# Kernel optimization log

Hardware: AMD Instinct MI355X
Metric: run time of the kernel (lower is better)

The kernel has to match this reference:

```python
import jax, jax.numpy as jnp
import numpy as np
from jax import lax

IMG = 800.0
PRE_NMS = 2000
POST_NMS = 1000
IOU_T = 0.7
BBOX_XFORM_CLIP = float(np.log(1000.0 / 16.0))


def build_anchors():
    # torchvision FPN anchor generator: one size per level, 3 aspect ratios
    strides = [4, 8, 16, 32, 64]
    sizes = [32, 64, 128, 256, 512]
    ratios = [0.5, 1.0, 2.0]
    out = []
    for s, sz in zip(strides, sizes):
        f = int(np.ceil(800 / s))  # feature map side
        base = []
        for r in ratios:
            w = sz * np.sqrt(1.0 / r)
            h = sz * np.sqrt(r)
            base.append([-w / 2, -h / 2, w / 2, h / 2])
        base = np.asarray(base)  # [3,4]
        sx = (np.arange(f) + 0.5) * s
        sy = (np.arange(f) + 0.5) * s
        yy, xx = np.meshgrid(sy, sx, indexing='ij')
        shifts = np.stack([xx, yy, xx, yy], -1).reshape(-1, 1, 4)
        out.append((shifts + base).reshape(-1, 4))
    return np.concatenate(out, 0).astype(np.float32)  # [159882,4]


def setup_inputs() -> dict:
    key = jax.random.key(0)
    k1, k2 = jax.random.split(key)
    B = 16
    anchors = jnp.asarray(build_anchors())
    A = anchors.shape[0]
    scores = jax.random.normal(k1, (B, A), dtype=jnp.float32)
    deltas = jax.random.normal(k2, (B, A, 4), dtype=jnp.float32) * 0.1
    return {"scores": scores, "deltas": deltas, "anchors": anchors}


def decode_boxes(deltas, anchors):
    wa = anchors[:, 2] - anchors[:, 0]
    ha = anchors[:, 3] - anchors[:, 1]
    cxa = anchors[:, 0] + 0.5 * wa
    cya = anchors[:, 1] + 0.5 * ha
    dx, dy = deltas[:, 0], deltas[:, 1]
    dw = jnp.minimum(deltas[:, 2], BBOX_XFORM_CLIP)
    dh = jnp.minimum(deltas[:, 3], BBOX_XFORM_CLIP)
    cx = dx * wa + cxa
    cy = dy * ha + cya
    w = jnp.exp(dw) * wa
    h = jnp.exp(dh) * ha
    boxes = jnp.stack([cx - 0.5 * w, cy - 0.5 * h, cx + 0.5 * w, cy + 0.5 * h], -1)
    return jnp.clip(boxes, 0.0, IMG)


def box_iou(a, b):
    # a: [N,4], b: [M,4]
    area_a = (a[:, 2] - a[:, 0]) * (a[:, 3] - a[:, 1])
    area_b = (b[:, 2] - b[:, 0]) * (b[:, 3] - b[:, 1])
    lt = jnp.maximum(a[:, None, :2], b[None, :, :2])
    rb = jnp.minimum(a[:, None, 2:], b[None, :, 2:])
    wh = jnp.clip(rb - lt, 0.0)
    inter = wh[..., 0] * wh[..., 1]
    return inter / (area_a[:, None] + area_b[None, :] - inter + 1e-9)


def greedy_nms_keep(boxes, iou_t):
    # boxes are sorted by descending score
    K = boxes.shape[0]
    iou = box_iou(boxes, boxes)  # [K,K]
    idx = jnp.arange(K)

    def body(i, keep):
        sup = (iou[i] > iou_t) & keep[i] & (idx > i)
        return keep & ~sup

    return lax.fori_loop(0, K, body, jnp.ones((K,), bool))


def _process_image(scores_i, deltas_i, anchors):
    # top-k pre-NMS on objectness logits (torchvision RPN order)
    top_logits, idx = lax.top_k(scores_i, PRE_NMS)
    boxes = decode_boxes(deltas_i[idx], anchors[idx])  # [PRE,4]
    keep = greedy_nms_keep(boxes, IOU_T)
    masked = jnp.where(keep, top_logits, -jnp.inf)
    kept_logits, idx2 = lax.top_k(masked, POST_NMS)
    kept_boxes = boxes[idx2]
    valid = jnp.isfinite(kept_logits)
    probs = jax.nn.sigmoid(jnp.where(valid, kept_logits, 0.0))
    out_boxes = jnp.where(valid[:, None], kept_boxes, 0.0)
    out_scores = jnp.where(valid, probs, 0.0)
    return jnp.concatenate([out_boxes, out_scores[:, None]], -1)  # [POST,5]


def reference(scores, deltas, anchors):
    return jax.vmap(_process_image, in_axes=(0, 0, None))(scores, deltas, anchors)
```

## Files before the change

### kernel.cpp

```cpp
#include <hip/hip_runtime.h>
#include <math.h>

#define PRE_NMS 2000
#define POST_NMS 1000
#define IOU_T 0.7f
#define IMGSZ 800.0f
#define CAP 6144
#define SORTN 2048
#define NBINS 1024
#define NWORDS 32
#define NSLICE 16
#define MROWS 2048

typedef unsigned long long u64;

__device__ __forceinline__ unsigned key_of(float f) {
    unsigned u = __float_as_uint(f);
    return (u & 0x80000000u) ? ~u : (u | 0x80000000u);
}
__device__ __forceinline__ float inv_key(unsigned k) {
    unsigned u = (k & 0x80000000u) ? (k ^ 0x80000000u) : ~k;
    return __uint_as_float(u);
}

__global__ __launch_bounds__(256) void hist_kernel(
    const float* __restrict__ scores, int A, unsigned* __restrict__ ghist) {
  int b = blockIdx.x, slice = blockIdx.y;
  __shared__ unsigned h[NBINS];
  int tid = threadIdx.x;
  for (int i = tid; i < NBINS; i += 256) h[i] = 0;
  __syncthreads();
  int per = (A + NSLICE - 1) / NSLICE;
  int lo = slice * per, hi = min(lo + per, A);
  const float* sc = scores + (size_t)b * A;
  for (int i = lo + tid; i < hi; i += 256)
    atomicAdd(&h[key_of(sc[i]) >> 22], 1u);
  __syncthreads();
  for (int i = tid; i < NBINS; i += 256)
    if (h[i]) atomicAdd(&ghist[b * NBINS + i], h[i]);
}

__global__ __launch_bounds__(256) void compact_kernel(
    const float* __restrict__ scores, int A, const unsigned* __restrict__ ghist,
    u64* __restrict__ cand, int* __restrict__ cand_cnt, int* __restrict__ T1) {
  int b = blockIdx.x, slice = blockIdx.y;
  int tid = threadIdx.x;
  int lane = tid & 63, wave = tid >> 6;
  __shared__ unsigned sa[2][NBINS];
  __shared__ int sT;
  for (int i = tid; i < NBINS; i += 256) sa[0][i] = ghist[b * NBINS + i];
  __syncthreads();
  int src = 0;
  for (int d = 1; d < NBINS; d <<= 1) {
    for (int i = tid; i < NBINS; i += 256)
      sa[src ^ 1][i] = sa[src][i] + ((i + d < NBINS) ? sa[src][i + d] : 0u);
    __syncthreads();
    src ^= 1;
  }
  for (int i = tid; i < NBINS; i += 256) {
    unsigned v = sa[src][i];
    unsigned nx = (i < NBINS - 1) ? sa[src][i + 1] : 0u;
    if (v >= PRE_NMS && nx < PRE_NMS) sT = i;
  }
  __syncthreads();
  int T = sT;
  if (slice == 0 && tid == 0) T1[b] = T;
  int per = (A + NSLICE - 1) / NSLICE;
  int lo = slice * per, hi = min(lo + per, A);
  const float* sc = scores + (size_t)b * A;
  int cnt = 0;
  for (int i = lo + tid; i < hi; i += 256)
    cnt += ((int)(key_of(sc[i]) >> 22) >= T);
  int pfx = cnt;
  #pragma unroll
  for (int d = 1; d < 64; d <<= 1) {
    int t2 = __shfl_up(pfx, d, 64);
    if (lane >= d) pfx += t2;
  }
  __shared__ int s_wt[4];
  __shared__ int s_base;
  if (lane == 63) s_wt[wave] = pfx;
  __syncthreads();
  if (tid == 0) {
    int tot = s_wt[0] + s_wt[1] + s_wt[2] + s_wt[3];
    int acc = 0;
    #pragma unroll
    for (int w2 = 0; w2 < 4; ++w2) { int t3 = s_wt[w2]; s_wt[w2] = acc; acc += t3; }
    s_base = atomicAdd(&cand_cnt[b], tot);
  }
  __syncthreads();
  int my_off = s_base + s_wt[wave] + (pfx - cnt);
  u64* cb = cand + (size_t)b * CAP;
  for (int i = lo + tid; i < hi; i += 256) {
    unsigned k = key_of(sc[i]);
    if ((int)(k >> 22) >= T) {
      if (my_off < CAP) cb[my_off] = ((u64)k << 32) | (unsigned)(~i);
      my_off++;
    }
  }
}

__global__ __launch_bounds__(1024) void refine_select_kernel(
    const u64* __restrict__ cand, const int* __restrict__ cand_cnt,
    const int* __restrict__ T1,
    u64* __restrict__ gsel, int* __restrict__ sel_cnt) {
  int b = blockIdx.x, tid = threadIdx.x;
  int lane = tid & 63;
  __shared__ unsigned h2[NBINS];
  __shared__ unsigned tmp[NBINS];
  __shared__ int s_above, s_sel, s_T2;
  int n = min(cand_cnt[b], CAP);
  const u64* cb = cand + (size_t)b * CAP;
  h2[tid] = 0;
  if (tid == 0) { s_above = 0; s_sel = 0; }
  __syncthreads();
  int T1v = T1[b];
  int loc = 0;
  for (int i = tid; i < n; i += 1024) {
    unsigned k = (unsigned)(cb[i] >> 32);
    if ((int)(k >> 22) > T1v) loc++;
    else atomicAdd(&h2[(k >> 12) & 1023], 1u);
  }
  for (int d = 32; d; d >>= 1) loc += __shfl_down(loc, d, 64);
  if (lane == 0 && loc) atomicAdd(&s_above, loc);
  __syncthreads();
  unsigned v = h2[tid];
  for (int d = 1; d < NBINS; d <<= 1) {
    tmp[tid] = v;
    __syncthreads();
    if (tid + d < NBINS) v += tmp[tid + d];
    __syncthreads();
  }
  tmp[tid] = v;
  __syncthreads();
  int above = s_above;
  unsigned nextv = (tid < NBINS - 1) ? tmp[tid + 1] : 0u;
  if (above + (int)v >= PRE_NMS && above + (int)nextv < PRE_NMS) s_T2 = tid;
  __syncthreads();
  unsigned thresh20 = ((unsigned)T1v << 10) | (unsigned)s_T2;
  u64* gs = gsel + (size_t)b * SORTN;
  for (int i = tid; i < n; i += 1024) {
    u64 cv = cb[i];
    if ((unsigned)(cv >> 44) >= thresh20) {
      int pos = atomicAdd(&s_sel, 1);
      if (pos < SORTN) gs[pos] = cv;
    }
  }
  __syncthreads();
  if (tid == 0) sel_cnt[b] = min(s_sel, SORTN);
}

__global__ __launch_bounds__(256) void rank_decode_kernel(
    const u64* __restrict__ gsel, const int* __restrict__ sel_cnt,
    const float* __restrict__ deltas, const float* __restrict__ anchors, int A,
    float* __restrict__ boxes, float* __restrict__ topk_logit) {
  int b = blockIdx.x, ci = blockIdx.y;
  int tid = threadIdx.x;
  __shared__ u64 keys[SORTN];
  __shared__ int s_part[256];
  const u64* gs = gsel + (size_t)b * SORTN;
  int n = sel_cnt[b];
  for (int i = tid; i < SORTN; i += 256)
    keys[i] = (i < n) ? gs[i] : 0ULL;
  __syncthreads();
  int half = tid >> 7;
  int li = tid & 127;
  int i = ci * 128 + li;
  u64 my = keys[i];
  int rank = 0;
  const ulonglong2* k2 = (const ulonglong2*)(keys + half * (SORTN / 2));
  #pragma unroll 4
  for (int j = 0; j < SORTN / 4; ++j) {
    ulonglong2 kk = k2[j];
    rank += (kk.x > my) + (kk.y > my);
  }
  s_part[tid] = rank;
  __syncthreads();
  if (half == 0) {
    rank = s_part[tid] + s_part[tid + 128];
    if (i < n && rank < PRE_NMS) {
      int a = (int)(~(unsigned)my);
      topk_logit[b * PRE_NMS + rank] = inv_key((unsigned)(my >> 32));
      const float CLIP = 4.135166556742356f;
      float4 dl = ((const float4*)deltas)[(size_t)b * A + a];
      float4 an = ((const float4*)anchors)[a];
      float wa = __fsub_rn(an.z, an.x);
      float ha = __fsub_rn(an.w, an.y);
      float cxa = __fadd_rn(an.x, __fmul_rn(0.5f, wa));
      float cya = __fadd_rn(an.y, __fmul_rn(0.5f, ha));
      float dw = fminf(dl.z, CLIP), dh = fminf(dl.w, CLIP);
      float cx = __fadd_rn(__fmul_rn(dl.x, wa), cxa);
      float cy = __fadd_rn(__fmul_rn(dl.y, ha), cya);
      float w2 = __fmul_rn((float)exp((double)dw), wa);
      float h2f = __fmul_rn((float)exp((double)dh), ha);
      float x1 = __fsub_rn(cx, __fmul_rn(0.5f, w2));
      float y1 = __fsub_rn(cy, __fmul_rn(0.5f, h2f));
      float x2 = __fadd_rn(cx, __fmul_rn(0.5f, w2));
      float y2 = __fadd_rn(cy, __fmul_rn(0.5f, h2f));
      x1 = fminf(fmaxf(x1, 0.f), IMGSZ);
      y1 = fminf(fmaxf(y1, 0.f), IMGSZ);
      x2 = fminf(fmaxf(x2, 0.f), IMGSZ);
      y2 = fminf(fmaxf(y2, 0.f), IMGSZ);
      ((float4*)boxes)[(size_t)b * PRE_NMS + rank] = make_float4(x1, y1, x2, y2);
    }
  }
}

__global__ __launch_bounds__(64) void iou_tile(
    const float* __restrict__ boxes, u64* __restrict__ maskT) {
  int k = blockIdx.x;
  int b = blockIdx.y;
  int wj = (int)((sqrtf(8.0f * k + 1.0f) - 1.0f) * 0.5f);
  while ((wj + 1) * (wj + 2) / 2 <= k) ++wj;
  while (wj * (wj + 1) / 2 > k) --wj;
  int ti = k - wj * (wj + 1) / 2;
  int lane = threadIdx.x;
  int i = ti * 64 + lane;
  const float4* bb = (const float4*)boxes + (size_t)b * PRE_NMS;
  __shared__ float4 sbox[64];
  int jg = wj * 64 + lane;
  sbox[lane] = bb[min(jg, PRE_NMS - 1)];
  float4 A4 = bb[min(i, PRE_NMS - 1)];
  __syncthreads();
  float area_a = __fmul_rn(__fsub_rn(A4.z, A4.x), __fsub_rn(A4.w, A4.y));
  u64 m = 0;
  #pragma unroll 8
  for (int jj = 0; jj < 64; ++jj) {
    float4 Bb = sbox[jj];
    float area_b = __fmul_rn(__fsub_rn(Bb.z, Bb.x), __fsub_rn(Bb.w, Bb.y));
    float ltx = fmaxf(A4.x, Bb.x), lty = fmaxf(A4.y, Bb.y);
    float rbx = fminf(A4.z, Bb.z), rby = fminf(A4.w, Bb.w);
    float iw = fmaxf(__fsub_rn(rbx, ltx), 0.f);
    float ih = fmaxf(__fsub_rn(rby, lty), 0.f);
    float inter = __fmul_rn(iw, ih);
    float denom = __fadd_rn(__fsub_rn(__fadd_rn(area_a, area_b), inter), 1e-9f);
    float iou = inter / denom;
    int j = wj * 64 + jj;
    if (j > i && iou > IOU_T) m |= 1ULL << jj;
  }
  maskT[((size_t)b * NWORDS + wj) * MROWS + i] = m;
}

#define WSTRIDE 65
#define BAR_LDS() asm volatile("s_waitcnt lgkmcnt(0)\n\ts_barrier" ::: "memory")
__global__ __launch_bounds__(256, 1) void nms_scan(
    const u64* __restrict__ maskT, const float* __restrict__ boxes,
    const float* __restrict__ logits, float* __restrict__ out) {
  int b = blockIdx.x;
  int tid = threadIdx.x;
  int wave = tid >> 6, lane = tid & 63;
  __shared__ u64 buf[3][NWORDS * WSTRIDE];
  __shared__ u64 s_keep[NWORDS];
  __shared__ u64 s_cur[2];
  if (tid < NWORDS) s_keep[tid] = (tid == NWORDS - 1) ? 0xFFFFULL : ~0ULL;
  const u64* mb = maskT + (size_t)b * NWORDS * MROWS;
  int w = tid >> 3;
  int sub = tid & 7;
  uint4 nx0, nx1, nx2, nx3;
  {
    const uint4* src = (const uint4*)(mb + (size_t)w * MROWS + sub * 8);
    uint4 a0 = src[0], a1 = src[1], a2 = src[2], a3 = src[3];
    u64* dst = &buf[0][w * WSTRIDE + sub * 8];
    dst[0] = ((u64)a0.y << 32) | a0.x;  dst[1] = ((u64)a0.w << 32) | a0.z;
    dst[2] = ((u64)a1.y << 32) | a1.x;  dst[3] = ((u64)a1.w << 32) | a1.z;
    dst[4] = ((u64)a2.y << 32) | a2.x;  dst[5] = ((u64)a2.w << 32) | a2.z;
    dst[6] = ((u64)a3.y << 32) | a3.x;  dst[7] = ((u64)a3.w << 32) | a3.z;
  }
  if (w >= 1) {
    const uint4* src = (const uint4*)(mb + (size_t)w * MROWS + 64 + sub * 8);
    nx0 = src[0]; nx1 = src[1]; nx2 = src[2]; nx3 = src[3];
  }
  BAR_LDS();
  for (int c = 0; c < NWORDS; ++c) {
    if (c + 1 < NWORDS && w >= c + 1) {
      u64* dst = &buf[(c + 1) % 3][w * WSTRIDE + sub * 8];
      dst[0] = ((u64)nx0.y << 32) | nx0.x;  dst[1] = ((u64)nx0.w << 32) | nx0.z;
      dst[2] = ((u64)nx1.y << 32) | nx1.x;  dst[3] = ((u64)nx1.w << 32) | nx1.z;
      dst[4] = ((u64)nx2.y << 32) | nx2.x;  dst[5] = ((u64)nx2.w << 32) | nx2.z;
      dst[6] = ((u64)nx3.y << 32) | nx3.x;  dst[7] = ((u64)nx3.w << 32) | nx3.z;
    }
    if (c + 2 < NWORDS && w >= c + 2) {
      const uint4* src = (const uint4*)(mb + (size_t)w * MROWS + (c + 2) * 64 + sub * 8);
      nx0 = src[0]; nx1 = src[1]; nx2 = src[2]; nx3 = src[3];
    }
    if (wave == 0) {
      u64 diag = buf[c % 3][c * WSTRIDE + lane];
      unsigned dlo = (unsigned)diag, dhi = (unsigned)(diag >> 32);
      u64 k0 = s_keep[c];
      unsigned clo = __builtin_amdgcn_readfirstlane((unsigned)k0);
      unsigned chi = __builtin_amdgcn_readfirstlane((unsigned)(k0 >> 32));
      #pragma unroll
      for (int bb = 0; bb < 32; ++bb) {
        unsigned rlo = __builtin_amdgcn_readlane(dlo, bb);
        unsigned rhi = __builtin_amdgcn_readlane(dhi, bb);
        unsigned msk = 0u - ((clo >> bb) & 1u);
        clo &= ~(rlo & msk);
        chi &= ~(rhi & msk);
      }
      #pragma unroll
      for (int bb = 0; bb < 32; ++bb) {
        unsigned rlo = __builtin_amdgcn_readlane(dlo, bb + 32);
        unsigned rhi = __builtin_amdgcn_readlane(dhi, bb + 32);
        unsigned msk = 0u - ((chi >> bb) & 1u);
        clo &= ~(rlo & msk);
        chi &= ~(rhi & msk);
      }
      u64 cur = ((u64)chi << 32) | clo;
      if (lane == 0) { s_keep[c] = cur; s_cur[c & 1] = cur; }
      if (c + 1 < NWORDS) {
        u64 row = buf[c % 3][(c + 1) * WSTRIDE + lane];
        u64 bit = (cur >> lane) & 1ULL;
        u64 v = row & (0ULL - bit);
        v |= __shfl_xor(v, 1, 64);
        v |= __shfl_xor(v, 2, 64);
        v |= __shfl_xor(v, 4, 64);
        v |= __shfl_xor(v, 8, 64);
        v |= __shfl_xor(v, 16, 64);
        v |= __shfl_xor(v, 32, 64);
        if (lane == 0 && v) atomicAnd(&s_keep[c + 1], ~v);
      }
    } else if (c >= 1) {
      u64 kept = s_cur[(c - 1) & 1];
      int g = lane >> 3, s = lane & 7;
      const u64* bbuf = &buf[(c - 1) % 3][0];
      for (int idx = (wave - 1) + 3 * g; idx < NWORDS - 1 - c; idx += 24) {
        int w2 = c + 1 + idx;
        u64 v = 0;
        #pragma unroll
        for (int k = 0; k < 8; ++k) {
          int r = s + 8 * k;
          u64 bit = (kept >> r) & 1ULL;
          v |= bbuf[w2 * WSTRIDE + r] & (0ULL - bit);
        }
        v |= __shfl_xor(v, 1, 64);
        v |= __shfl_xor(v, 2, 64);
        v |= __shfl_xor(v, 4, 64);
        if (s == 0 && v) atomicAnd(&s_keep[w2], ~v);
      }
    }
    BAR_LDS();
  }
  __shared__ int pre[NWORDS];
  __shared__ int s_tot;
  if (tid == 0) {
    int acc = 0;
    for (int ww = 0; ww < NWORDS; ++ww) {
      pre[ww] = acc;
      acc += __popcll(s_keep[ww]);
    }
    s_tot = acc;
  }
  __syncthreads();
  const float* lg_b = logits + b * PRE_NMS;
  const float4* bx_b = (const float4*)boxes + (size_t)b * PRE_NMS;
  for (int i = tid; i < PRE_NMS; i += 256) {
    u64 wv = s_keep[i >> 6];
    if ((wv >> (i & 63)) & 1) {
      int rank = pre[i >> 6] + __popcll(wv & ((1ULL << (i & 63)) - 1ULL));
      if (rank < POST_NMS) {
        float4 bx = bx_b[i];
        float lg = lg_b[i];
        float e = (float)exp(-(double)lg);
        float pp = 1.0f / (1.0f + e);
        float* o = out + ((size_t)b * POST_NMS + rank) * 5;
        o[0] = bx.x; o[1] = bx.y; o[2] = bx.z; o[3] = bx.w; o[4] = pp;
      }
    }
  }
  int tot = s_tot;
  for (int j = tid; j < POST_NMS; j += 256) {
    if (j >= tot) {
      float* o = out + ((size_t)b * POST_NMS + j) * 5;
      o[0] = 0.f; o[1] = 0.f; o[2] = 0.f; o[3] = 0.f; o[4] = 0.f;
    }
  }
}

extern "C" void kernel_launch(void* const* d_in, const int* in_sizes, int n_in,
                              void* d_out, int out_size, void* d_ws, size_t ws_size,
                              hipStream_t stream) {
  const float* scores  = (const float*)d_in[0];
  const float* deltas  = (const float*)d_in[1];
  const float* anchors = (const float*)d_in[2];
  int A = in_sizes[2] / 4;
  int B = in_sizes[0] / A;

  char* ws = (char*)d_ws;
  size_t off = 0;
  auto alloc = [&](size_t bytes) {
    void* p = ws + off;
    off += (bytes + 255) & ~(size_t)255;
    return p;
  };
  unsigned* ghist    = (unsigned*)alloc((size_t)B * NBINS * 4);
  int*      cand_cnt = (int*)alloc((size_t)B * 4);
  size_t zero_bytes = off;
  int*      T1       = (int*)alloc((size_t)B * 4);
  u64*      cand     = (u64*)alloc((size_t)B * CAP * 8);
  u64*      gsel     = (u64*)alloc((size_t)B * SORTN * 8);
  int*      sel_cnt  = (int*)alloc((size_t)B * 4);
  float*    topk_lg  = (float*)alloc((size_t)B * PRE_NMS * 4);
  float*    boxes    = (float*)alloc((size_t)B * PRE_NMS * 16);
  u64*      maskT    = (u64*)alloc((size_t)B * NWORDS * MROWS * 8);

  hipMemsetAsync(ws, 0, zero_bytes, stream);

  hist_kernel<<<dim3(B, NSLICE), 256, 0, stream>>>(scores, A, ghist);
  compact_kernel<<<dim3(B, NSLICE), 256, 0, stream>>>(scores, A, ghist, cand, cand_cnt, T1);
  refine_select_kernel<<<B, 1024, 0, stream>>>(cand, cand_cnt, T1, gsel, sel_cnt);
  rank_decode_kernel<<<dim3(B, SORTN / 128), 256, 0, stream>>>(
      gsel, sel_cnt, deltas, anchors, A, boxes, topk_lg);
  int ntiles = NWORDS * (NWORDS + 1) / 2;
  iou_tile<<<dim3(ntiles, B), 64, 0, stream>>>(boxes, maskT);
  nms_scan<<<B, 256, 0, stream>>>(maskT, boxes, topk_lg, (float*)d_out);
}
```

Baseline: 225.1 us.

## Skip empty IoU mask tiles in NMS scan using per-tile occupancy flags

The IoU tile kernel now writes a per-tile flag saying whether any bit in the 64x64 suppression tile is set. The NMS scan loads these flags into shared memory and uses them to skip global loads of empty tiles, the serial diagonal readlane reduction, and the off-diagonal OR-reductions. This aims to cut memory traffic and serial work on the latency-bound scan, since most tiles of random boxes are empty. It adds an extra flag buffer, its writes, and flag lookups in the inner loop.

```diff
diff --git a/kernel.cpp b/kernel.cpp
--- a/kernel.cpp
+++ b/kernel.cpp
@@ -11,6 +11,7 @@
 #define NWORDS 32
 #define NSLICE 16
 #define MROWS 2048
+#define NTILES 528
 
 typedef unsigned long long u64;
 
@@ -207,7 +208,8 @@
 }
 
 __global__ __launch_bounds__(64) void iou_tile(
-    const float* __restrict__ boxes, u64* __restrict__ maskT) {
+    const float* __restrict__ boxes, u64* __restrict__ maskT,
+    unsigned* __restrict__ tflag) {
   int k = blockIdx.x;
   int b = blockIdx.y;
   int wj = (int)((sqrtf(8.0f * k + 1.0f) - 1.0f) * 0.5f);
@@ -239,12 +241,15 @@
     if (j > i && iou > IOU_T) m |= 1ULL << jj;
   }
   maskT[((size_t)b * NWORDS + wj) * MROWS + i] = m;
+  u64 anyb = __ballot(m != 0ULL);
+  if (lane == 0) tflag[(size_t)b * NTILES + k] = (anyb != 0ULL) ? 1u : 0u;
 }
 
 #define WSTRIDE 65
 #define BAR_LDS() asm volatile("s_waitcnt lgkmcnt(0)\n\ts_barrier" ::: "memory")
 __global__ __launch_bounds__(256, 1) void nms_scan(
-    const u64* __restrict__ maskT, const float* __restrict__ boxes,
+    const u64* __restrict__ maskT, const unsigned* __restrict__ tflag,
+    const float* __restrict__ boxes,
     const float* __restrict__ logits, float* __restrict__ out) {
   int b = blockIdx.x;
   int tid = threadIdx.x;
@@ -252,6 +257,10 @@
   __shared__ u64 buf[3][NWORDS * WSTRIDE];
   __shared__ u64 s_keep[NWORDS];
   __shared__ u64 s_cur[2];
+  __shared__ unsigned char sflag[NTILES];
+  const unsigned* tf = tflag + (size_t)b * NTILES;
+  for (int i2 = tid; i2 < NTILES; i2 += 256)
+    sflag[i2] = (unsigned char)(tf[i2] != 0u);
   if (tid < NWORDS) s_keep[tid] = (tid == NWORDS - 1) ? 0xFFFFULL : ~0ULL;
   const u64* mb = maskT + (size_t)b * NWORDS * MROWS;
   int w = tid >> 3;
@@ -266,48 +275,57 @@
     dst[4] = ((u64)a2.y << 32) | a2.x;  dst[5] = ((u64)a2.w << 32) | a2.z;
     dst[6] = ((u64)a3.y << 32) | a3.x;  dst[7] = ((u64)a3.w << 32) | a3.z;
   }
-  if (w >= 1) {
+  bool have = (w >= 1);
+  if (have) {
     const uint4* src = (const uint4*)(mb + (size_t)w * MROWS + 64 + sub * 8);
     nx0 = src[0]; nx1 = src[1]; nx2 = src[2]; nx3 = src[3];
   }
   BAR_LDS();
   for (int c = 0; c < NWORDS; ++c) {
-    if (c + 1 < NWORDS && w >= c + 1) {
+    if (c + 1 < NWORDS && have) {
       u64* dst = &buf[(c + 1) % 3][w * WSTRIDE + sub * 8];
       dst[0] = ((u64)nx0.y << 32) | nx0.x;  dst[1] = ((u64)nx0.w << 32) | nx0.z;
       dst[2] = ((u64)nx1.y << 32) | nx1.x;  dst[3] = ((u64)nx1.w << 32) | nx1.z;
       dst[4] = ((u64)nx2.y << 32) | nx2.x;  dst[5] = ((u64)nx2.w << 32) | nx2.z;
       dst[6] = ((u64)nx3.y << 32) | nx3.x;  dst[7] = ((u64)nx3.w << 32) | nx3.z;
     }
-    if (c + 2 < NWORDS && w >= c + 2) {
+    have = false;
+    if (c + 2 < NWORDS && w >= c + 2 &&
+        sflag[(w * (w + 1)) / 2 + (c + 2)]) {
       const uint4* src = (const uint4*)(mb + (size_t)w * MROWS + (c + 2) * 64 + sub * 8);
       nx0 = src[0]; nx1 = src[1]; nx2 = src[2]; nx3 = src[3];
+      have = true;
     }
     if (wave == 0) {
-      u64 diag = buf[c % 3][c * WSTRIDE + lane];
-      unsigned dlo = (unsigned)diag, dhi = (unsigned)(diag >> 32);
       u64 k0 = s_keep[c];
-      unsigned clo = __builtin_amdgcn_readfirstlane((unsigned)k0);
-      unsigned chi = __builtin_amdgcn_readfirstlane((unsigned)(k0 >> 32));
-      #pragma unroll
-      for (int bb = 0; bb < 32; ++bb) {
-        unsigned rlo = __builtin_amdgcn_readlane(dlo, bb);
-        unsigned rhi = __builtin_amdgcn_readlane(dhi, bb);
-        unsigned msk = 0u - ((clo >> bb) & 1u);
-        clo &= ~(rlo & msk);
-        chi &= ~(rhi & msk);
+      u64 cur;
+      if (sflag[(c * (c + 3)) >> 1]) {
+        u64 diag = buf[c % 3][c * WSTRIDE + lane];
+        unsigned dlo = (unsigned)diag, dhi = (unsigned)(diag >> 32);
+        unsigned clo = __builtin_amdgcn_readfirstlane((unsigned)k0);
+        unsigned chi = __builtin_amdgcn_readfirstlane((unsigned)(k0 >> 32));
+        #pragma unroll
+        for (int bb = 0; bb < 32; ++bb) {
+          unsigned rlo = __builtin_amdgcn_readlane(dlo, bb);
+          unsigned rhi = __builtin_amdgcn_readlane(dhi, bb);
+          unsigned msk = 0u - ((clo >> bb) & 1u);
+          clo &= ~(rlo & msk);
+          chi &= ~(rhi & msk);
+        }
+        #pragma unroll
+        for (int bb = 0; bb < 32; ++bb) {
+          unsigned rlo = __builtin_amdgcn_readlane(dlo, bb + 32);
+          unsigned rhi = __builtin_amdgcn_readlane(dhi, bb + 32);
+          unsigned msk = 0u - ((chi >> bb) & 1u);
+          clo &= ~(rlo & msk);
+          chi &= ~(rhi & msk);
+        }
+        cur = ((u64)chi << 32) | clo;
+      } else {
+        cur = k0;
       }
-      #pragma unroll
-      for (int bb = 0; bb < 32; ++bb) {
-        unsigned rlo = __builtin_amdgcn_readlane(dlo, bb + 32);
-        unsigned rhi = __builtin_amdgcn_readlane(dhi, bb + 32);
-        unsigned msk = 0u - ((chi >> bb) & 1u);
-        clo &= ~(rlo & msk);
-        chi &= ~(rhi & msk);
-      }
-      u64 cur = ((u64)chi << 32) | clo;
       if (lane == 0) { s_keep[c] = cur; s_cur[c & 1] = cur; }
-      if (c + 1 < NWORDS) {
+      if (c + 1 < NWORDS && sflag[(((c + 1) * (c + 2)) >> 1) + c]) {
         u64 row = buf[c % 3][(c + 1) * WSTRIDE + lane];
         u64 bit = (cur >> lane) & 1ULL;
         u64 v = row & (0ULL - bit);
@@ -325,6 +343,7 @@
       const u64* bbuf = &buf[(c - 1) % 3][0];
       for (int idx = (wave - 1) + 3 * g; idx < NWORDS - 1 - c; idx += 24) {
         int w2 = c + 1 + idx;
+        if (!sflag[(w2 * (w2 + 1)) / 2 + (c - 1)]) continue;
         u64 v = 0;
         #pragma unroll
         for (int k = 0; k < 8; ++k) {
@@ -402,6 +421,7 @@
   float*    topk_lg  = (float*)alloc((size_t)B * PRE_NMS * 4);
   float*    boxes    = (float*)alloc((size_t)B * PRE_NMS * 16);
   u64*      maskT    = (u64*)alloc((size_t)B * NWORDS * MROWS * 8);
+  unsigned* tflag    = (unsigned*)alloc((size_t)B * NTILES * 4);
 
   hipMemsetAsync(ws, 0, zero_bytes, stream);
 
@@ -410,7 +430,7 @@
   refine_select_kernel<<<B, 1024, 0, stream>>>(cand, cand_cnt, T1, gsel, sel_cnt);
   rank_decode_kernel<<<dim3(B, SORTN / 128), 256, 0, stream>>>(
       gsel, sel_cnt, deltas, anchors, A, boxes, topk_lg);
-  int ntiles = NWORDS * (NWORDS + 1) / 2;
-  iou_tile<<<dim3(ntiles, B), 64, 0, stream>>>(boxes, maskT);
-  nms_scan<<<B, 256, 0, stream>>>(maskT, boxes, topk_lg, (float*)d_out);
-}
+  int ntiles = NTILES;
+  iou_tile<<<dim3(ntiles, B), 64, 0, stream>>>(boxes, maskT, tflag);
+  nms_scan<<<B, 256, 0, stream>>>(maskT, tflag, boxes, topk_lg, (float*)d_out);
+}
```

Result: faster. 204.3 us (-9.3%).
